# Kernel optimization log

Measured on AMD Instinct MI355X. Metric: run time of the kernel, lower is better.

Reference implementation:

```python
import jax, jax.numpy as jnp
import numpy as np

B, C, H, W = 32, 128, 32, 32
E, K, D, HID = 16, 2, 128, 512  # nbExperts, topK, nbIn=nbOut, hidden=4*max(nbIn,nbOut)


def setup_inputs() -> dict:
    key = jax.random.key(0)
    ks = jax.random.split(key, 6)
    init = lambda k, shape, fan: (jax.random.normal(k, shape, jnp.float32) / np.sqrt(fan)).astype(jnp.float32)
    return {
        "x": jax.random.normal(ks[0], (B, C, H, W), jnp.float32),
        "gate_w": init(ks[1], (D, E), D),
        "gate_b": jnp.zeros((E,), jnp.float32),
        "noise_w": init(ks[2], (D, E), D),
        "noise_b": jnp.zeros((E,), jnp.float32),
        "w1": init(ks[3], (E, D, HID), D),
        "b1": jnp.zeros((E, HID), jnp.float32),
        "w2": init(ks[4], (E, HID, D), HID),
        "b2": jnp.zeros((E, D), jnp.float32),
        "top_k": K,
    }


def reference(x, gate_w, gate_b, noise_w, noise_b, w1, b1, w2, b2, top_k):
    b, c, h, w = x.shape
    xt = x.transpose(0, 2, 3, 1).reshape(-1, c)  # [T, D] tokens (fromCNN path)
    T = xt.shape[0]

    # --- GatingWithNoise: gate(x) + randn * softplus(noise(x)) ---
    logits = xt @ gate_w + gate_b                      # [T, E]
    noise_sd = jax.nn.softplus(xt @ noise_w + noise_b)  # [T, E]
    noise = jax.random.normal(jax.random.key(42), logits.shape, logits.dtype)
    logits = logits + noise * noise_sd

    # --- top-k, softmax over k, scatter to dense [T, E] gate matrix ---
    top_vals, top_idx = jax.lax.top_k(logits, top_k)   # [T, K]
    probs = jax.nn.softmax(top_vals, axis=1)           # [T, K]
    gates = jnp.zeros((T, E), x.dtype).at[jnp.arange(T)[:, None], top_idx].set(probs)

    # --- dense path: run every expert, weighted combine ---
    hdn = jax.nn.relu(jnp.einsum('td,edh->teh', xt, w1) + b1)  # [T, E, HID]
    eo = jnp.einsum('teh,ehd->ted', hdn, w2) + b2              # [T, E, D]
    out = jnp.einsum('te,ted->td', gates, eo)                  # [T, D]

    out = out.reshape(b, h, w, c).transpose(0, 3, 1, 2)        # back to NCHW
    gates = gates.reshape(b, h, w, E)
    return out, gates
```

## Files before the change

### kernel.cpp

```cpp
#include <hip/hip_runtime.h>
#include <stdint.h>

#define NB       32
#define NC       128
#define NHW      1024
#define NT       32768
#define NE       16
#define NHID     512
#define NGBLK    512

typedef __attribute__((ext_vector_type(8))) short short8v;
typedef __attribute__((ext_vector_type(4))) float f32x4;

__device__ __forceinline__ unsigned short f2bf(float f) {
    uint32_t u = __float_as_uint(f);
    uint32_t r = u + 0x7fffu + ((u >> 16) & 1u);
    return (unsigned short)(r >> 16);
}
__device__ __forceinline__ float bf2f(unsigned short u) {
    return __uint_as_float(((uint32_t)u) << 16);
}

__device__ __forceinline__ void gll16(const void* g, void* l) {
    __builtin_amdgcn_global_load_lds(
        (const __attribute__((address_space(1))) uint32_t*)g,
        (__attribute__((address_space(3))) uint32_t*)l, 16, 0, 0);
}

#define WAIT_VM4_LGKM0() asm volatile("s_waitcnt vmcnt(4) lgkmcnt(0)" ::: "memory")
#define WAIT_VM4()       asm volatile("s_waitcnt vmcnt(4)" ::: "memory")
#define WAIT_VM0()       asm volatile("s_waitcnt vmcnt(0)" ::: "memory")
#define WAIT_LGKM()      asm volatile("s_waitcnt lgkmcnt(0)" ::: "memory")
#define SBAR()           { asm volatile("" ::: "memory"); __builtin_amdgcn_s_barrier(); asm volatile("" ::: "memory"); }

__device__ __forceinline__ uint32_t rotl32(uint32_t x, uint32_t d) {
    return (x << d) | (x >> (32u - d));
}

__device__ __forceinline__ void threefry2x32_20(uint32_t k0, uint32_t k1,
                                                uint32_t& x0, uint32_t& x1) {
    const uint32_t ks0 = k0, ks1 = k1, ks2 = k0 ^ k1 ^ 0x1BD11BDAu;
    x0 += ks0; x1 += ks1;
#define TFR(r) { x0 += x1; x1 = rotl32(x1, r); x1 ^= x0; }
    TFR(13u) TFR(15u) TFR(26u) TFR(6u)
    x0 += ks1; x1 += ks2 + 1u;
    TFR(17u) TFR(29u) TFR(16u) TFR(24u)
    x0 += ks2; x1 += ks0 + 2u;
    TFR(13u) TFR(15u) TFR(26u) TFR(6u)
    x0 += ks0; x1 += ks1 + 3u;
    TFR(17u) TFR(29u) TFR(16u) TFR(24u)
    x0 += ks1; x1 += ks2 + 4u;
    TFR(13u) TFR(15u) TFR(26u) TFR(6u)
    x0 += ks2; x1 += ks0 + 5u;
#undef TFR
}

__device__ __forceinline__ float erfinv_xla_f32(float x) {
    float w = -log1pf(-x * x);
    float p;
    if (w < 5.0f) {
        w = w - 2.5f;
        p = 2.81022636e-08f;
        p = fmaf(p, w, 3.43273939e-07f);
        p = fmaf(p, w, -3.5233877e-06f);
        p = fmaf(p, w, -4.39150654e-06f);
        p = fmaf(p, w, 0.00021858087f);
        p = fmaf(p, w, -0.00125372503f);
        p = fmaf(p, w, -0.00417768164f);
        p = fmaf(p, w, 0.246640727f);
        p = fmaf(p, w, 1.50140941f);
    } else {
        w = sqrtf(w) - 3.0f;
        p = -0.000200214257f;
        p = fmaf(p, w, 0.000100950558f);
        p = fmaf(p, w, 0.00134934322f);
        p = fmaf(p, w, -0.00367342844f);
        p = fmaf(p, w, 0.00573950773f);
        p = fmaf(p, w, -0.0076224613f);
        p = fmaf(p, w, 0.00943887047f);
        p = fmaf(p, w, 1.00167406f);
        p = fmaf(p, w, 2.83297682f);
    }
    return p * x;
}

__device__ __forceinline__ float jax_noise_elem(uint32_t i) {
    uint32_t x0 = 0u, x1 = i;
    threefry2x32_20(0u, 42u, x0, x1);
    uint32_t bits = x0 ^ x1;
    float f = __uint_as_float(0x3f800000u | (bits >> 9)) - 1.0f;
    const float lo = -0.99999994f;
    float u = f * 2.0f + lo;
    u = fmaxf(lo, u);
    return 1.41421354f * erfinv_xla_f32(u);
}

__global__ __launch_bounds__(256) void moe_gate_tw_kernel(
    const float* __restrict__ x,
    const float* __restrict__ gate_w, const float* __restrict__ gate_b,
    const float* __restrict__ noise_w, const float* __restrict__ noise_b,
    float* __restrict__ gates_out,
    int*   __restrict__ top_idx,
    float* __restrict__ top_prob,
    int*   __restrict__ rank,
    int*   __restrict__ bcnt,
    unsigned short* __restrict__ xtb,
    const float* __restrict__ w1, unsigned short* __restrict__ w1bt,
    const float* __restrict__ w2, unsigned short* __restrict__ w2bt,
    int do_new)
{
    __shared__ union { float lw[32 * 160]; float ts[64][65]; } sm;
    __shared__ int lcnt[16];

    const int tid = threadIdx.x;

    if (blockIdx.x >= NGBLK) {
        int blk = blockIdx.x - NGBLK;
        const float* src;  unsigned short* dst;  int R, C;
        if (blk < 256) { src = w1; dst = w1bt; R = 128; C = 512; }
        else           { src = w2; dst = w2bt; R = 512; C = 128; blk -= 256; }
        const int nr = R >> 6, ncc = C >> 6;
        const int e = blk / (nr * ncc);
        const int rem = blk % (nr * ncc);
        const int rt = rem / ncc, ct = rem % ncc;
        const float* S = src + (size_t)e * R * C + (size_t)(rt * 64) * C + ct * 64;
        unsigned short* D = dst + (size_t)e * R * C + (size_t)(ct * 64) * R + rt * 64;
        #pragma unroll
        for (int i = 0; i < 16; ++i) {
            int lin = i * 256 + tid;
            int r = lin >> 6, c = lin & 63;
            sm.ts[r][c] = S[(size_t)r * C + c];
        }
        __syncthreads();
        #pragma unroll
        for (int i = 0; i < 16; ++i) {
            int lin = i * 256 + tid;
            int c = lin >> 6, r = lin & 63;
            D[(size_t)c * R + r] = f2bf(sm.ts[r][c]);
        }
        return;
    }

    const int tl  = tid >> 2;
    const int q   = tid & 3;
    const int t   = blockIdx.x * 64 + tl;
    const int b   = t >> 10, hw = t & 1023;

    if (tid < 16) lcnt[tid] = 0;

    for (int idx = tid; idx < 4096; idx += 256) {
        int ci = idx >> 7;
        int r  = idx & 127;
        int qq = r >> 5, e = r & 31;
        int c  = qq * 32 + ci;
        float v = (e < 16) ? gate_w[c * 16 + e] : noise_w[c * 16 + (e - 16)];
        sm.lw[ci * 160 + qq * 40 + e] = v;
    }
    __syncthreads();

    float acc[32];
    #pragma unroll
    for (int e = 0; e < 32; ++e) acc[e] = 0.f;

    unsigned short xh[32];
    const float* xq = x + (size_t)b * (NC * NHW) + (size_t)(q * 32) * NHW + hw;
    const float* wq = sm.lw + q * 40;
    #pragma unroll 4
    for (int ci = 0; ci < 32; ++ci) {
        float xv = xq[(size_t)ci << 10];
        xh[ci] = f2bf(xv);
        const f32x4* wr = (const f32x4*)(wq + ci * 160);
        #pragma unroll
        for (int j = 0; j < 8; ++j) {
            f32x4 w4 = wr[j];
            #pragma unroll
            for (int k = 0; k < 4; ++k)
                acc[j * 4 + k] = fmaf(xv, w4[k], acc[j * 4 + k]);
        }
    }

    if (do_new) {
        #pragma unroll
        for (int j = 0; j < 4; ++j) {
            short8v v;
            #pragma unroll
            for (int k = 0; k < 8; ++k) v[k] = (short)xh[j * 8 + k];
            *(short8v*)(xtb + (size_t)t * 128 + q * 32 + j * 8) = v;
        }
    }

    #pragma unroll
    for (int e = 0; e < 32; ++e) {
        acc[e] += __shfl_xor(acc[e], 1);
        acc[e] += __shfl_xor(acc[e], 2);
    }

    float lg[4];
    #pragma unroll
    for (int j = 0; j < 4; ++j) {
        int e = q * 4 + j;
        float g  = acc[e] + gate_b[e];
        float an = acc[16 + e] + noise_b[e];
        float sd = fmaxf(an, 0.f) + log1pf(expf(-fabsf(an)));
        float nz = jax_noise_elem((uint32_t)t * 16u + (uint32_t)e);
        lg[j] = fmaf(nz, sd, g);
    }

    float v1 = lg[0], v2 = -INFINITY;
    int   i1 = q * 4, i2 = 0x7fffffff;
    #pragma unroll
    for (int j = 1; j < 4; ++j) {
        float v = lg[j]; int e = q * 4 + j;
        if (v > v1) { v2 = v1; i2 = i1; v1 = v; i1 = e; }
        else if (v > v2) { v2 = v; i2 = e; }
    }
    #pragma unroll
    for (int m = 1; m <= 2; m <<= 1) {
        float pv1 = __shfl_xor(v1, m), pv2 = __shfl_xor(v2, m);
        int   pi1 = __shfl_xor(i1, m), pi2 = __shfl_xor(i2, m);
        bool pBest = (pv1 > v1) || (pv1 == v1 && pi1 < i1);
        float c2v; int c2i;
        if (pBest) { c2v = v1;  c2i = i1;  v1 = pv1; i1 = pi1;
                     if (!((c2v > pv2) || (c2v == pv2 && c2i < pi2))) { c2v = pv2; c2i = pi2; }
        } else     { c2v = pv1; c2i = pi1;
                     if (!((c2v > v2)  || (c2v == v2  && c2i < i2)))  { c2v = v2;  c2i = i2;  }
        }
        v2 = c2v; i2 = c2i;
    }

    float qq = expf(v2 - v1);
    float s  = 1.0f + qq;
    float p1 = 1.0f / s;
    float p2 = qq / s;

    f32x4 g4;
    #pragma unroll
    for (int j = 0; j < 4; ++j) {
        int e = q * 4 + j;
        g4[j] = (e == i1) ? p1 : ((e == i2) ? p2 : 0.f);
    }
    *(f32x4*)(gates_out + (size_t)t * 16 + q * 4) = g4;

    if (q == 0) {
        top_idx[t * 2 + 0] = i1;  top_idx[t * 2 + 1] = i2;
        top_prob[t * 2 + 0] = p1; top_prob[t * 2 + 1] = p2;
        if (do_new) {
            int r1 = atomicAdd(&lcnt[i1], 1);
            int r2 = atomicAdd(&lcnt[i2], 1);
            rank[t * 2 + 0] = r1;
            rank[t * 2 + 1] = r2;
        }
    }
    if (do_new) {
        __syncthreads();
        if (tid < 16) bcnt[blockIdx.x * 16 + tid] = lcnt[tid];
    }
}

__global__ __launch_bounds__(256) void scan_kernel(
    const int* __restrict__ bcnt,
    int* __restrict__ poff, int* __restrict__ blk2e,
    int* __restrict__ blk2chunk, int* __restrict__ total_chunks,
    int* __restrict__ bbase,
    int* __restrict__ pair_tok)
{
    __shared__ int ps[16][17];
    __shared__ int gb[16][17];
    __shared__ int scnt[16];
    __shared__ int snch[16];
    __shared__ int scum[17];
    __shared__ int spoff[16];
    const int tid = threadIdx.x;
    const int e = tid >> 4, g = tid & 15;

    int s = 0;
    for (int b = g * 32; b < g * 32 + 32; ++b)
        s += bcnt[b * 16 + e];
    ps[e][g] = s;
    __syncthreads();

    if (tid < 16) {
        int run = 0;
        for (int gg = 0; gg < 16; ++gg) { gb[tid][gg] = run; run += ps[tid][gg]; }
        scnt[tid] = run;
        snch[tid] = (run + 127) >> 7;
    }
    __syncthreads();

    if (tid == 0) {
        int cc = 0, off = 0;
        for (int ee = 0; ee < 16; ++ee) {
            scum[ee] = cc; spoff[ee] = off;
            cc += snch[ee]; off += snch[ee] << 7;
        }
        scum[16] = cc;
        *total_chunks = cc;
    }
    __syncthreads();
    const int tot = scum[16];
    for (int idx = tid; idx < tot; idx += 256) {
        int ee = 0;
        #pragma unroll
        for (int k = 0; k < 15; ++k)
            if (idx >= scum[k + 1]) ee = k + 1;
        blk2e[idx] = ee;
        blk2chunk[idx] = idx - scum[ee];
    }
    if (tid < 16) poff[tid] = spoff[tid];

    {
        int run = spoff[e] + gb[e][g];
        for (int b = g * 32; b < g * 32 + 32; ++b) {
            bbase[b * 16 + e] = run;
            run += bcnt[b * 16 + e];
        }
    }

    for (int ee = 0; ee < 16; ++ee) {
        int start = spoff[ee] + scnt[ee];
        int end   = spoff[ee] + (snch[ee] << 7);
        for (int i = start + tid; i < end; i += 256)
            pair_tok[i] = -1;
    }
}

__global__ __launch_bounds__(256) void scatter_kernel(
    const int* __restrict__ top_idx, const int* __restrict__ rank,
    const int* __restrict__ bbase, int* __restrict__ pair_tok,
    int* __restrict__ slot_of)
{
    int i = blockIdx.x * 256 + threadIdx.x;
    int t = i >> 1;
    int e = top_idx[i];
    int slot = bbase[(t >> 6) * 16 + e] + rank[i];
    pair_tok[slot] = t;
    slot_of[i] = slot;
}

__device__ __forceinline__ void stage_w1(const unsigned short* w1e, short* W1s,
                                         int hcn, int wid, int lane) {
    #pragma unroll
    for (int k2 = 0; k2 < 4; ++k2) {
        int i2 = wid * 4 + k2;
        int r2 = i2 * 4 + (lane >> 4);
        int s2 = lane & 15;
        gll16(w1e + (size_t)(hcn + r2) * 128 + ((s2 ^ (r2 & 15)) * 8),
              W1s + i2 * 512);
    }
}
__device__ __forceinline__ void stage_w2(const unsigned short* w2e, short* W2s,
                                         int hcn, int wid, int lane) {
    #pragma unroll
    for (int k2 = 0; k2 < 4; ++k2) {
        int i2 = wid * 4 + k2;
        int r2 = i2 * 8 + (lane >> 3);
        int s2 = lane & 7;
        gll16(w2e + (size_t)r2 * 512 + hcn + ((s2 ^ (r2 & 7)) * 8),
              W2s + i2 * 512);
    }
}

__global__ __launch_bounds__(256, 2) void moe_mfma_kernel(
    const unsigned short* __restrict__ xtb,
    const int* __restrict__ pair_tok, const int* __restrict__ blk2e,
    const int* __restrict__ blk2chunk, const int* __restrict__ poff,
    const int* __restrict__ total_chunks,
    const unsigned short* __restrict__ w1bt,
    const float* __restrict__ b1,
    const unsigned short* __restrict__ w2bt,
    const float* __restrict__ b2,
    unsigned short* __restrict__ pair_y)
{
    __shared__ short Hs[128 * 64];
    __shared__ short W1s[64 * 128];
    __shared__ short W2s[128 * 64];

    const int blk = (blockIdx.x & 7) * 66 + (blockIdx.x >> 3);
    if (blk >= *total_chunks) return;
    const int e  = blk2e[blk];
    const int p0 = poff[e] + (blk2chunk[blk] << 7);
    const int tid  = threadIdx.x;
    const int lane = tid & 63;
    const int wid  = tid >> 6;
    const int wm   = wid >> 1;
    const int wn   = wid & 1;
    const int l16  = lane & 15;
    const int lg   = lane >> 4;

    const unsigned short* w1e = w1bt + (size_t)e * 512 * 128;
    const unsigned short* w2e = w2bt + (size_t)e * 128 * 512;

    stage_w1(w1e, W1s, 0, wid, lane);
    stage_w2(w2e, W2s, 0, wid, lane);

    short8v xa[4][4];
    #pragma unroll
    for (int af = 0; af < 4; ++af) {
        int row = wm * 64 + af * 16 + l16;
        int tok = pair_tok[p0 + row];
        #pragma unroll
        for (int kk = 0; kk < 4; ++kk) {
            short8v v = {};
            if (tok >= 0)
                v = *(const short8v*)(xtb + (size_t)tok * 128 + kk * 32 + lg * 8);
            xa[af][kk] = v;
        }
    }

    f32x4 yacc[4][4];
    #pragma unroll
    for (int af = 0; af < 4; ++af)
        #pragma unroll
        for (int nj = 0; nj < 4; ++nj)
            yacc[af][nj] = (f32x4){0.f, 0.f, 0.f, 0.f};

    for (int c = 0; c < 8; ++c) {
        WAIT_VM4_LGKM0(); SBAR();

        f32x4 hacc[4][2];
        #pragma unroll
        for (int af = 0; af < 4; ++af)
            #pragma unroll
            for (int ni = 0; ni < 2; ++ni)
                hacc[af][ni] = (f32x4){0.f, 0.f, 0.f, 0.f};

        __builtin_amdgcn_s_setprio(1);
        #pragma unroll
        for (int kk = 0; kk < 4; ++kk) {
            int slot = kk * 4 + lg;
            #pragma unroll
            for (int ni = 0; ni < 2; ++ni) {
                int hr = wn * 32 + ni * 16 + l16;
                short8v bfr = *(const short8v*)(W1s + hr * 128 + ((slot ^ (hr & 15)) * 8));
                #pragma unroll
                for (int af = 0; af < 4; ++af)
                    hacc[af][ni] = __builtin_amdgcn_mfma_f32_16x16x32_bf16(
                        xa[af][kk], bfr, hacc[af][ni], 0, 0, 0);
            }
        }
        __builtin_amdgcn_s_setprio(0);

        #pragma unroll
        for (int ni = 0; ni < 2; ++ni) {
            int col = wn * 32 + ni * 16 + l16;
            float b1v = b1[e * 512 + (c << 6) + col];
            #pragma unroll
            for (int af = 0; af < 4; ++af) {
                #pragma unroll
                for (int r = 0; r < 4; ++r) {
                    int m = wm * 64 + af * 16 + lg * 4 + r;
                    float v = fmaxf(hacc[af][ni][r] + b1v, 0.f);
                    Hs[m * 64 + (((col >> 3) ^ (m & 7)) << 3) + (col & 7)] = (short)f2bf(v);
                }
            }
        }
        WAIT_LGKM(); SBAR();

        if (c < 7) { stage_w1(w1e, W1s, (c + 1) << 6, wid, lane); WAIT_VM4(); }
        else       { WAIT_VM0(); }
        SBAR();

        __builtin_amdgcn_s_setprio(1);
        #pragma unroll
        for (int kk = 0; kk < 2; ++kk) {
            int slot = kk * 4 + lg;
            short8v ha[4];
            #pragma unroll
            for (int af = 0; af < 4; ++af) {
                int row = wm * 64 + af * 16 + l16;
                ha[af] = *(const short8v*)(Hs + row * 64 + ((slot ^ (row & 7)) * 8));
            }
            #pragma unroll
            for (int nj = 0; nj < 4; ++nj) {
                int dr = wn * 64 + nj * 16 + l16;
                short8v bfr = *(const short8v*)(W2s + dr * 64 + ((slot ^ (dr & 7)) * 8));
                #pragma unroll
                for (int af = 0; af < 4; ++af)
                    yacc[af][nj] = __builtin_amdgcn_mfma_f32_16x16x32_bf16(
                        ha[af], bfr, yacc[af][nj], 0, 0, 0);
            }
        }
        __builtin_amdgcn_s_setprio(0);
        WAIT_LGKM(); SBAR();

        if (c < 7) stage_w2(w2e, W2s, (c + 1) << 6, wid, lane);
    }

    #pragma unroll
    for (int nj = 0; nj < 4; ++nj) {
        int d = wn * 64 + nj * 16 + l16;
        float b2v = b2[e * 128 + d];
        #pragma unroll
        for (int af = 0; af < 4; ++af) {
            #pragma unroll
            for (int r = 0; r < 4; ++r) {
                int m = wm * 64 + af * 16 + lg * 4 + r;
                pair_y[(size_t)(p0 + m) * 128 + d] = f2bf(yacc[af][nj][r] + b2v);
            }
        }
    }
}

__global__ __launch_bounds__(256) void combine_kernel(
    const unsigned short* __restrict__ pair_y, const int* __restrict__ slot_of,
    const float* __restrict__ top_prob, float* __restrict__ out)
{
    __shared__ float ob[64][129];
    const int blk = blockIdx.x;
    const int b = blk >> 4;
    const int hw0 = (blk & 15) << 6;
    const int tid = threadIdx.x;
    #pragma unroll
    for (int i = 0; i < 4; ++i) {
        int lin = i * 256 + tid;
        int tl = lin >> 4, dg = lin & 15;
        int t = b * 1024 + hw0 + tl;
        int s0 = slot_of[t * 2], s1 = slot_of[t * 2 + 1];
        float p0 = top_prob[t * 2], p1 = top_prob[t * 2 + 1];
        short8v y0 = *(const short8v*)(pair_y + (size_t)s0 * 128 + dg * 8);
        short8v y1 = *(const short8v*)(pair_y + (size_t)s1 * 128 + dg * 8);
        #pragma unroll
        for (int j = 0; j < 8; ++j)
            ob[tl][dg * 8 + j] = p0 * bf2f((unsigned short)y0[j]) + p1 * bf2f((unsigned short)y1[j]);
    }
    __syncthreads();
    #pragma unroll
    for (int i = 0; i < 32; ++i) {
        int lin = i * 256 + tid;
        int d = lin >> 6, hwl = lin & 63;
        out[((size_t)b * 128 + d) * 1024 + hw0 + hwl] = ob[hwl][d];
    }
}

__global__ __launch_bounds__(256) void moe_expert_kernel(
    const float* __restrict__ x,
    const int* __restrict__ top_idx, const float* __restrict__ top_prob,
    const float* __restrict__ w1, const float* __restrict__ b1,
    const float* __restrict__ w2, const float* __restrict__ b2,
    float* __restrict__ out)
{
    __shared__ float xsB[128];
    __shared__ float hb[512];

    const int tid = threadIdx.x;
    const int t = blockIdx.x;
    const int b = t >> 10, hw = t & 1023;

    if (tid < 128)
        xsB[tid] = x[((size_t)b * 128 + tid) * NHW + hw];
    __syncthreads();

    float oacc = 0.f;
    #pragma unroll
    for (int k = 0; k < 2; ++k) {
        const int e = top_idx[t * 2 + k];
        const float pw = top_prob[t * 2 + k];
        const float* W1 = w1 + (size_t)e * (128 * 512);
        float a0 = 0.f, a1 = 0.f;
        for (int d = 0; d < 128; ++d) {
            float xv = xsB[d];
            a0 = fmaf(xv, W1[d * 512 + tid], a0);
            a1 = fmaf(xv, W1[d * 512 + tid + 256], a1);
        }
        hb[tid]       = fmaxf(a0 + b1[e * 512 + tid], 0.f);
        hb[tid + 256] = fmaxf(a1 + b1[e * 512 + tid + 256], 0.f);
        __syncthreads();
        if (tid < 128) {
            const float* W2 = w2 + (size_t)e * (512 * 128);
            float a = 0.f;
            for (int h = 0; h < 512; ++h)
                a = fmaf(hb[h], W2[h * 128 + tid], a);
            oacc = fmaf(pw, a + b2[e * 128 + tid], oacc);
        }
        __syncthreads();
    }
    if (tid < 128)
        out[((size_t)b * 128 + tid) * NHW + hw] = oacc;
}

extern "C" void kernel_launch(void* const* d_in, const int* in_sizes, int n_in,
                              void* d_out, int out_size, void* d_ws, size_t ws_size,
                              hipStream_t stream) {
    const float* x       = (const float*)d_in[0];
    const float* gate_w  = (const float*)d_in[1];
    const float* gate_b  = (const float*)d_in[2];
    const float* noise_w = (const float*)d_in[3];
    const float* noise_b = (const float*)d_in[4];
    const float* w1      = (const float*)d_in[5];
    const float* b1      = (const float*)d_in[6];
    const float* w2      = (const float*)d_in[7];
    const float* b2      = (const float*)d_in[8];

    float* out   = (float*)d_out;
    float* gates = out + (size_t)NB * NC * NHW;

    const size_t OFF_POFF   = 0;
    const size_t OFF_TOTAL  = 1024;
    const size_t OFF_B2E    = 4096;
    const size_t OFF_B2C    = 8192;
    const size_t OFF_TIDX   = 12288;
    const size_t OFF_RANK   = OFF_TIDX  + (size_t)NT * 2 * 4;
    const size_t OFF_SLOT   = OFF_RANK  + (size_t)NT * 2 * 4;
    const size_t OFF_PROB   = OFF_SLOT  + (size_t)NT * 2 * 4;
    const size_t OFF_BCNT   = OFF_PROB  + (size_t)NT * 2 * 4;
    const size_t OFF_BBASE  = OFF_BCNT  + (size_t)NGBLK * 16 * 4;
    const size_t OFF_XTB    = OFF_BBASE + (size_t)NGBLK * 16 * 4;
    const size_t OFF_W1BT   = OFF_XTB   + (size_t)NT * 128 * 2;
    const size_t OFF_W2BT   = OFF_W1BT  + (size_t)NE * 512 * 128 * 2;
    const size_t OFF_PTOK   = OFF_W2BT  + (size_t)NE * 128 * 512 * 2;
    const size_t NPAIR_PAD  = 67584;
    const size_t OFF_PAIRY  = OFF_PTOK  + NPAIR_PAD * 4;
    const size_t NEED       = OFF_PAIRY + NPAIR_PAD * 128 * 2;

    char* ws = (char*)d_ws;
    int*   poff     = (int*)(ws + OFF_POFF);
    int*   total_ch = (int*)(ws + OFF_TOTAL);
    int*   blk2e    = (int*)(ws + OFF_B2E);
    int*   blk2c    = (int*)(ws + OFF_B2C);
    int*   top_idx  = (int*)(ws + OFF_TIDX);
    int*   rank     = (int*)(ws + OFF_RANK);
    int*   slot_of  = (int*)(ws + OFF_SLOT);
    float* top_prob = (float*)(ws + OFF_PROB);
    int*   bcnt     = (int*)(ws + OFF_BCNT);
    int*   bbase    = (int*)(ws + OFF_BBASE);
    unsigned short* xtb    = (unsigned short*)(ws + OFF_XTB);
    unsigned short* w1bt   = (unsigned short*)(ws + OFF_W1BT);
    unsigned short* w2bt   = (unsigned short*)(ws + OFF_W2BT);
    int*   pair_tok = (int*)(ws + OFF_PTOK);
    unsigned short* pair_y = (unsigned short*)(ws + OFF_PAIRY);

    const int use_new = (ws_size >= NEED) ? 1 : 0;

    moe_gate_tw_kernel<<<use_new ? (NGBLK + 512) : NGBLK, 256, 0, stream>>>(
        x, gate_w, gate_b, noise_w, noise_b,
        gates, top_idx, top_prob, rank, bcnt, xtb,
        w1, w1bt, w2, w2bt, use_new);

    if (use_new) {
        scan_kernel<<<1, 256, 0, stream>>>(bcnt, poff, blk2e, blk2c, total_ch,
                                           bbase, pair_tok);
        scatter_kernel<<<NT * 2 / 256, 256, 0, stream>>>(top_idx, rank, bbase,
                                                         pair_tok, slot_of);
        moe_mfma_kernel<<<528, 256, 0, stream>>>(
            xtb, pair_tok, blk2e, blk2c, poff, total_ch,
            w1bt, b1, w2bt, b2, pair_y);
        combine_kernel<<<512, 256, 0, stream>>>(pair_y, slot_of, top_prob, out);
    } else {
        moe_expert_kernel<<<NT, 256, 0, stream>>>(
            x, top_idx, top_prob, w1, b1, w2, b2, out);
    }
}
```

Before: 100.0 us.

## Double-buffer expert weight tiles and split MoE GEMM across 8 waves

Doubles the block to 512 threads with each wave handling 32 token rows, and double-buffers W1/W2 LDS tiles so the next hidden chunk's weights are prefetched during compute of the current chunk. One barrier per chunk is removed. The change aims to hide global-load latency and raise the number of waves in flight, at the cost of more LDS per block (possibly lower block occupancy) and less register reuse of B fragments per wave.

```diff
diff --git a/kernel.cpp b/kernel.cpp
--- a/kernel.cpp
+++ b/kernel.cpp
@@ -28,8 +28,7 @@
 }
 
 #define WAIT_VM4_LGKM0() asm volatile("s_waitcnt vmcnt(4) lgkmcnt(0)" ::: "memory")
-#define WAIT_VM4()       asm volatile("s_waitcnt vmcnt(4)" ::: "memory")
-#define WAIT_VM0()       asm volatile("s_waitcnt vmcnt(0)" ::: "memory")
+#define WAIT_VM0_LGKM0() asm volatile("s_waitcnt vmcnt(0) lgkmcnt(0)" ::: "memory")
 #define WAIT_LGKM()      asm volatile("s_waitcnt lgkmcnt(0)" ::: "memory")
 #define SBAR()           { asm volatile("" ::: "memory"); __builtin_amdgcn_s_barrier(); asm volatile("" ::: "memory"); }
 
@@ -340,8 +339,8 @@
 __device__ __forceinline__ void stage_w1(const unsigned short* w1e, short* W1s,
                                          int hcn, int wid, int lane) {
     #pragma unroll
-    for (int k2 = 0; k2 < 4; ++k2) {
-        int i2 = wid * 4 + k2;
+    for (int k2 = 0; k2 < 2; ++k2) {
+        int i2 = wid * 2 + k2;
         int r2 = i2 * 4 + (lane >> 4);
         int s2 = lane & 15;
         gll16(w1e + (size_t)(hcn + r2) * 128 + ((s2 ^ (r2 & 15)) * 8),
@@ -351,8 +350,8 @@
 __device__ __forceinline__ void stage_w2(const unsigned short* w2e, short* W2s,
                                          int hcn, int wid, int lane) {
     #pragma unroll
-    for (int k2 = 0; k2 < 4; ++k2) {
-        int i2 = wid * 4 + k2;
+    for (int k2 = 0; k2 < 2; ++k2) {
+        int i2 = wid * 2 + k2;
         int r2 = i2 * 8 + (lane >> 3);
         int s2 = lane & 7;
         gll16(w2e + (size_t)r2 * 512 + hcn + ((s2 ^ (r2 & 7)) * 8),
@@ -360,7 +359,7 @@
     }
 }
 
-__global__ __launch_bounds__(256, 2) void moe_mfma_kernel(
+__global__ __launch_bounds__(512, 4) void moe_mfma_kernel(
     const unsigned short* __restrict__ xtb,
     const int* __restrict__ pair_tok, const int* __restrict__ blk2e,
     const int* __restrict__ blk2chunk, const int* __restrict__ poff,
@@ -372,8 +371,8 @@
     unsigned short* __restrict__ pair_y)
 {
     __shared__ short Hs[128 * 64];
-    __shared__ short W1s[64 * 128];
-    __shared__ short W2s[128 * 64];
+    __shared__ short W1s[2][64 * 128];
+    __shared__ short W2s[2][128 * 64];
 
     const int blk = (blockIdx.x & 7) * 66 + (blockIdx.x >> 3);
     if (blk >= *total_chunks) return;
@@ -390,13 +389,10 @@
     const unsigned short* w1e = w1bt + (size_t)e * 512 * 128;
     const unsigned short* w2e = w2bt + (size_t)e * 128 * 512;
 
-    stage_w1(w1e, W1s, 0, wid, lane);
-    stage_w2(w2e, W2s, 0, wid, lane);
-
-    short8v xa[4][4];
-    #pragma unroll
-    for (int af = 0; af < 4; ++af) {
-        int row = wm * 64 + af * 16 + l16;
+    short8v xa[2][4];
+    #pragma unroll
+    for (int af = 0; af < 2; ++af) {
+        int row = wm * 32 + af * 16 + l16;
         int tok = pair_tok[p0 + row];
         #pragma unroll
         for (int kk = 0; kk < 4; ++kk) {
@@ -407,19 +403,34 @@
         }
     }
 
-    f32x4 yacc[4][4];
-    #pragma unroll
-    for (int af = 0; af < 4; ++af)
+    stage_w1(w1e, W1s[0], 0, wid, lane);
+    stage_w2(w2e, W2s[0], 0, wid, lane);
+    stage_w1(w1e, W1s[1], 64, wid, lane);
+    stage_w2(w2e, W2s[1], 64, wid, lane);
+
+    f32x4 yacc[2][4];
+    #pragma unroll
+    for (int af = 0; af < 2; ++af)
         #pragma unroll
         for (int nj = 0; nj < 4; ++nj)
             yacc[af][nj] = (f32x4){0.f, 0.f, 0.f, 0.f};
 
+    const int rowA0 = wm * 32 + l16, rowA1 = rowA0 + 16;
+
     for (int c = 0; c < 8; ++c) {
-        WAIT_VM4_LGKM0(); SBAR();
-
-        f32x4 hacc[4][2];
-        #pragma unroll
-        for (int af = 0; af < 4; ++af)
+        const short* W1b = W1s[c & 1];
+        const short* W2b = W2s[c & 1];
+
+        if (c >= 1 && c <= 6) {
+            stage_w1(w1e, W1s[(c + 1) & 1], (c + 1) << 6, wid, lane);
+            stage_w2(w2e, W2s[(c + 1) & 1], (c + 1) << 6, wid, lane);
+        }
+        if (c <= 6) { WAIT_VM4_LGKM0(); } else { WAIT_VM0_LGKM0(); }
+        SBAR();
+
+        f32x4 hacc[2][2];
+        #pragma unroll
+        for (int af = 0; af < 2; ++af)
             #pragma unroll
             for (int ni = 0; ni < 2; ++ni)
                 hacc[af][ni] = (f32x4){0.f, 0.f, 0.f, 0.f};
@@ -431,9 +442,9 @@
             #pragma unroll
             for (int ni = 0; ni < 2; ++ni) {
                 int hr = wn * 32 + ni * 16 + l16;
-                short8v bfr = *(const short8v*)(W1s + hr * 128 + ((slot ^ (hr & 15)) * 8));
+                short8v bfr = *(const short8v*)(W1b + hr * 128 + ((slot ^ (hr & 15)) * 8));
                 #pragma unroll
-                for (int af = 0; af < 4; ++af)
+                for (int af = 0; af < 2; ++af)
                     hacc[af][ni] = __builtin_amdgcn_mfma_f32_16x16x32_bf16(
                         xa[af][kk], bfr, hacc[af][ni], 0, 0, 0);
             }
@@ -445,10 +456,10 @@
             int col = wn * 32 + ni * 16 + l16;
             float b1v = b1[e * 512 + (c << 6) + col];
             #pragma unroll
-            for (int af = 0; af < 4; ++af) {
+            for (int af = 0; af < 2; ++af) {
                 #pragma unroll
                 for (int r = 0; r < 4; ++r) {
-                    int m = wm * 64 + af * 16 + lg * 4 + r;
+                    int m = wm * 32 + af * 16 + lg * 4 + r;
                     float v = fmaxf(hacc[af][ni][r] + b1v, 0.f);
                     Hs[m * 64 + (((col >> 3) ^ (m & 7)) << 3) + (col & 7)] = (short)f2bf(v);
                 }
@@ -456,34 +467,22 @@
         }
         WAIT_LGKM(); SBAR();
 
-        if (c < 7) { stage_w1(w1e, W1s, (c + 1) << 6, wid, lane); WAIT_VM4(); }
-        else       { WAIT_VM0(); }
-        SBAR();
-
         __builtin_amdgcn_s_setprio(1);
         #pragma unroll
         for (int kk = 0; kk < 2; ++kk) {
             int slot = kk * 4 + lg;
-            short8v ha[4];
-            #pragma unroll
-            for (int af = 0; af < 4; ++af) {
-                int row = wm * 64 + af * 16 + l16;
-                ha[af] = *(const short8v*)(Hs + row * 64 + ((slot ^ (row & 7)) * 8));
-            }
+            short8v a0 = *(const short8v*)(Hs + rowA0 * 64 + ((slot ^ (rowA0 & 7)) * 8));
+            short8v a1 = *(const short8v*)(Hs + rowA1 * 64 + ((slot ^ (rowA1 & 7)) * 8));
             #pragma unroll
             for (int nj = 0; nj < 4; ++nj) {
                 int dr = wn * 64 + nj * 16 + l16;
-                short8v bfr = *(const short8v*)(W2s + dr * 64 + ((slot ^ (dr & 7)) * 8));
-                #pragma unroll
-                for (int af = 0; af < 4; ++af)
-                    yacc[af][nj] = __builtin_amdgcn_mfma_f32_16x16x32_bf16(
-                        ha[af], bfr, yacc[af][nj], 0, 0, 0);
+                short8v bfr = *(const short8v*)(W2b + dr * 64 + ((slot ^ (dr & 7)) * 8));
+                yacc[0][nj] = __builtin_amdgcn_mfma_f32_16x16x32_bf16(a0, bfr, yacc[0][nj], 0, 0, 0);
+                yacc[1][nj] = __builtin_amdgcn_mfma_f32_16x16x32_bf16(a1, bfr, yacc[1][nj], 0, 0, 0);
             }
         }
         __builtin_amdgcn_s_setprio(0);
         WAIT_LGKM(); SBAR();
-
-        if (c < 7) stage_w2(w2e, W2s, (c + 1) << 6, wid, lane);
     }
 
     #pragma unroll
@@ -491,10 +490,10 @@
         int d = wn * 64 + nj * 16 + l16;
         float b2v = b2[e * 128 + d];
         #pragma unroll
-        for (int af = 0; af < 4; ++af) {
+        for (int af = 0; af < 2; ++af) {
             #pragma unroll
             for (int r = 0; r < 4; ++r) {
-                int m = wm * 64 + af * 16 + lg * 4 + r;
+                int m = wm * 32 + af * 16 + lg * 4 + r;
                 pair_y[(size_t)(p0 + m) * 128 + d] = f2bf(yacc[af][nj][r] + b2v);
             }
         }
@@ -641,7 +640,7 @@
                                            bbase, pair_tok);
         scatter_kernel<<<NT * 2 / 256, 256, 0, stream>>>(top_idx, rank, bbase,
                                                          pair_tok, slot_of);
-        moe_mfma_kernel<<<528, 256, 0, stream>>>(
+        moe_mfma_kernel<<<528, 512, 0, stream>>>(
             xtb, pair_tok, blk2e, blk2c, poff, total_ch,
             w1bt, b1, w2bt, b2, pair_y);
         combine_kernel<<<512, 256, 0, stream>>>(pair_y, slot_of, top_prob, out);
```

Result: no change. 98.80 us (-1.2%).
